# Kernel tuning notes

Measured on AMD Instinct MI355X. Metric: run time of the kernel, lower is better.

The kernel has to match this reference:

```python
import jax, jax.numpy as jnp
import numpy as np

HW = 8   # window height
WW = 8   # window width
NH = 8   # num heads
N = HW * WW  # tokens per window
DIM = 128
KEXPAND = 2


def _rel_index():
    # Swin relative-position index, [N, N] ints in [0, (2*HW-1)*(2*WW-1))
    coords = np.stack(np.meshgrid(np.arange(HW), np.arange(WW), indexing='ij')).reshape(2, -1)
    rel = (coords[:, :, None] - coords[:, None, :]).transpose(1, 2, 0)  # [N,N,2]
    rel[..., 0] += HW - 1
    rel[..., 1] += WW - 1
    rel[..., 0] *= 2 * WW - 1
    return jnp.asarray(rel.sum(-1))


def setup_inputs() -> dict:
    key = jax.random.key(0)
    ks = jax.random.split(key, 13)
    b, h, w, c = 4, 256, 256, DIM
    inp = {
        'qq': jax.random.normal(ks[0], (b, h * w, c), jnp.float32),
        'kk': jax.random.normal(ks[1], (b, h * w, KEXPAND * c), jnp.float32),
        'vv': jax.random.normal(ks[2], (b, h * w, c), jnp.float32),
        'w_q': jax.random.normal(ks[3], (c, c), jnp.float32) * 0.02,
        'b_q': jnp.zeros((c,), jnp.float32),
        'w_k': jax.random.normal(ks[4], (KEXPAND * c, c), jnp.float32) * 0.02,
        'b_k': jnp.zeros((c,), jnp.float32),
        'w_v': jax.random.normal(ks[5], (c, c), jnp.float32) * 0.02,
        'b_v': jnp.zeros((c,), jnp.float32),
        'w_o': jax.random.normal(ks[6], (c, c), jnp.float32) * 0.02,
        'b_o': jnp.zeros((c,), jnp.float32),
        'bias_table': jax.random.normal(ks[7], ((2 * HW - 1) * (2 * WW - 1), NH), jnp.float32) * 0.02,
        'h': h,
        'w': w,
    }
    return inp


def reference(qq, kk, vv, w_q, b_q, w_k, b_k, w_v, b_v, w_o, b_o, bias_table, h, w):
    b, n, c = qq.shape
    hd = c // NH
    pad_b = (-h) % HW
    pad_r = (-w) % WW
    Hp, Wp = h + pad_b, w + pad_r

    def pad_img(x):
        ck = x.shape[-1]
        x = x.reshape(b, h, w, ck)
        return jnp.pad(x, ((0, 0), (0, pad_b), (0, pad_r), (0, 0)))

    # QKV projections (zero-padded regions become just the bias, same as torch)
    qp = pad_img(qq) @ w_q + b_q  # [b, Hp, Wp, c]
    kp = pad_img(kk) @ w_k + b_k
    vp = pad_img(vv) @ w_v + b_v

    def windows(x):
        x = x.reshape(b, Hp // HW, HW, Wp // WW, WW, c)
        x = x.transpose(0, 1, 3, 2, 4, 5).reshape(-1, N, NH, hd)
        return x.transpose(0, 2, 1, 3)  # [nw, NH, N, hd]

    q, k, v = windows(qp), windows(kp), windows(vp)

    scores = jnp.einsum('wnqd,wnkd->wnqk', q, k) / jnp.sqrt(jnp.asarray(hd, q.dtype))
    bias = bias_table[_rel_index().reshape(-1)].reshape(N, N, NH).transpose(2, 0, 1)  # [NH,N,N]
    attn = jax.nn.softmax(scores + bias[None], axis=-1)
    y = jnp.einsum('wnqk,wnkd->wnqd', attn, v)  # [nw, NH, N, hd]

    # merge heads and un-window
    y = y.transpose(0, 2, 1, 3).reshape(b, Hp // HW, Wp // WW, HW, WW, c)
    y = y.transpose(0, 1, 3, 2, 4, 5).reshape(b, Hp, Wp, c)
    out = y @ w_o + b_o
    out = out[:, :h, :w, :]
    return out.reshape(b, -1, c)
```

## Files before the change

### kernel.cpp

```cpp
#include <hip/hip_runtime.h>
#include <cstdint>

typedef float f32x4  __attribute__((ext_vector_type(4)));
typedef float f32x16 __attribute__((ext_vector_type(16)));
typedef short bf16x8 __attribute__((ext_vector_type(8)));
typedef unsigned int u32;

#define QP_BASE 0
#define KP_BASE 16384
#define VT_BASE 32768

__device__ __forceinline__ unsigned short f2bf(float f){
  union { float f; uint32_t u; } v; v.f = f;
  uint32_t u = v.u;
  return (unsigned short)((u + 0x7FFFu + ((u >> 16) & 1u)) >> 16);
}
__device__ __forceinline__ float bf2f(unsigned short h){
  union { uint32_t u; float f; } v; v.u = ((uint32_t)h) << 16;
  return v.f;
}
__device__ __forceinline__ u32 pack2bf(float a, float b){
  return (u32)f2bf(a) | ((u32)f2bf(b) << 16);
}
__device__ __forceinline__ f32x4 mfma16(bf16x8 a, bf16x8 b, f32x4 c){
  return __builtin_amdgcn_mfma_f32_16x16x32_bf16(a, b, c, 0, 0, 0);
}
__device__ __forceinline__ f32x16 mfma32(bf16x8 a, bf16x8 b, f32x16 c){
  return __builtin_amdgcn_mfma_f32_32x32x16_bf16(a, b, c, 0, 0, 0);
}
__device__ __forceinline__ void gload_lds16(const void* gsrc, void* ldst){
  __builtin_amdgcn_global_load_lds(
    (const __attribute__((address_space(1))) unsigned int*)gsrc,
    (__attribute__((address_space(3))) unsigned int*)ldst, 16, 0, 0);
}

__global__ void prep_kernel(const float* __restrict__ wq, const float* __restrict__ wk,
                            const float* __restrict__ wv, const float* __restrict__ wo,
                            const float* __restrict__ btab, unsigned short* __restrict__ wsu)
{
  const int idx = blockIdx.x * 256 + threadIdx.x;
  if (idx < 16384){
    const int n = idx >> 7, k = idx & 127;
    wsu[n*128 + (k ^ ((n & 7) << 3))] = f2bf(wq[k*128 + n]);
  } else if (idx < 32768){
    const int i = idx - 16384, n = i >> 7, k = i & 127;
    wsu[16384 + n*128 + (k ^ ((n & 7) << 3))] = f2bf(wv[k*128 + n]);
  } else if (idx < 65536){
    const int i = idx - 32768, n = i >> 8, k = i & 255;
    wsu[32768 + n*256 + (k ^ ((n & 7) << 3))] = f2bf(wk[k*128 + n]);
  } else if (idx < 81920){
    const int i = idx - 65536, n = i >> 7, k = i & 127;
    const float f = wo[k*128 + n];
    const unsigned short hv = f2bf(f);
    wsu[65536 + n*128 + k] = hv;
    wsu[81920 + n*128 + k] = f2bf(f - bf2f(hv));
  } else if (idx < 98304){
    const int i = idx - 81920;
    const int q  = i & 31;
    const int ib = (i >> 5) & 7;
    const int h5 = (i >> 8) & 1;
    const int t  = (i >> 9) & 1;
    const int qh = (i >> 10) & 1;
    const int h  = (i >> 11);
    const int qg = qh*32 + q;
    const int qi = qg >> 3, qj = qg & 7;
    u32 wv2 = 0;
#pragma unroll
    for (int e = 0; e < 2; ++e){
      const int r = 2*ib + e;
      const int key = t*32 + 4*h5 + (r & 3) + 8*(r >> 2);
      const int ki = key >> 3, kj = key & 7;
      const int rel = (qi - ki + 7) * 15 + (qj - kj + 7);
      wv2 |= ((u32)f2bf(btab[rel*8 + h])) << (16*e);
    }
    reinterpret_cast<u32*>(wsu + 98304)[i] = wv2;
  }
}

template<int KC, bool VT>
__device__ __forceinline__ void proj_one(const float* __restrict__ X, const float* __restrict__ bias,
    const char* wlds, char* outstage, long winbase, int wave, int lane, int g, int c16)
{
  constexpr int NKS = KC / 32;
  constexpr int SH  = (KC == 128) ? 8 : 9;
  const int rA = 16*wave + c16;
  const float* xrow = X + (winbase + (long)(rA >> 3) * 256 + (rA & 7)) * KC;
  bf16x8 a[NKS];
#pragma unroll
  for (int ks = 0; ks < NKS; ++ks){
    const float4* p = reinterpret_cast<const float4*>(xrow + 32*ks + 8*g);
    const float4 x0 = p[0], x1 = p[1];
    bf16x8 t;
    t[0]=(short)f2bf(x0.x); t[1]=(short)f2bf(x0.y); t[2]=(short)f2bf(x0.z); t[3]=(short)f2bf(x0.w);
    t[4]=(short)f2bf(x1.x); t[5]=(short)f2bf(x1.y); t[6]=(short)f2bf(x1.z); t[7]=(short)f2bf(x1.w);
    a[ks] = t;
  }
  f32x4 acc[8];
#pragma unroll
  for (int ct = 0; ct < 8; ++ct) acc[ct] = f32x4{0.f,0.f,0.f,0.f};
#pragma unroll
  for (int ct = 0; ct < 8; ++ct){
    const int n = ct*16 + c16;
#pragma unroll
    for (int ks = 0; ks < NKS; ++ks){
      const bf16x8 b = *reinterpret_cast<const bf16x8*>(
          wlds + ((n << SH) + (((32*ks + 8*g) << 1) ^ ((n & 7) << 4))));
      acc[ct] = mfma16(a[ks], b, acc[ct]);
    }
  }
#pragma unroll
  for (int ct = 0; ct < 8; ++ct){
    const float bsv = bias[ct*16 + c16];
#pragma unroll
    for (int r = 0; r < 4; ++r){
      const float v = acc[ct][r] + bsv;
      const unsigned short hv = f2bf(v);
      const int row = 16*wave + 4*g + r;
      int off;
      if (VT) off = (ct << 11) + (c16 << 7) + ((row << 1) ^ ((c16 & 7) << 4));
      else    off = (row << 8) + (((ct*16 + c16) << 1) ^ ((row & 15) << 4));
      *reinterpret_cast<unsigned short*>(outstage + off) = hv;
    }
  }
}

__global__ __launch_bounds__(256, 2) void proj_kernel(
    const float* __restrict__ qq, const float* __restrict__ kkin, const float* __restrict__ vvin,
    const float* __restrict__ b_q, const float* __restrict__ b_k, const float* __restrict__ b_v,
    const unsigned short* __restrict__ wsu,
    unsigned short* __restrict__ qs, unsigned short* __restrict__ ksg, unsigned short* __restrict__ vsg)
{
  __shared__ char smem[81920];
  const int tid = threadIdx.x;
  const int wave = tid >> 6, lane = tid & 63;
  const int g = lane >> 4, c16 = lane & 15;
  const bool isK = blockIdx.x >= 256;
  char* outstage = smem + 65536;

  const char* wsrc = reinterpret_cast<const char*>(wsu) + (isK ? 65536 : 0);
#pragma unroll
  for (int i = 0; i < 16; ++i){
    const int off = (wave*16 + i) * 1024;
    gload_lds16(wsrc + off + lane*16, smem + off);
  }
  __syncthreads();

  const int w0 = (isK ? (blockIdx.x - 256) : blockIdx.x) * 16;
  for (int wl = 0; wl < 16; ++wl){
    const int win = w0 + wl;
    const int bb = win >> 10, wy = (win >> 5) & 31, wx = win & 31;
    const long winbase = (long)bb * 65536 + (long)wy * 2048 + wx * 8;

    if (!isK){
      proj_one<128,false>(qq, b_q, smem, outstage, winbase, wave, lane, g, c16);
      asm volatile("s_waitcnt lgkmcnt(0)" ::: "memory");
      {
        char* dst = reinterpret_cast<char*>(qs) + (size_t)win * 16384 + wave*4096;
        const char* srcs = outstage + wave*4096;
#pragma unroll
        for (int i = 0; i < 4; ++i){
          const uint4 d = *reinterpret_cast<const uint4*>(srcs + i*1024 + lane*16);
          *reinterpret_cast<uint4*>(dst + i*1024 + lane*16) = d;
        }
      }
      __syncthreads();
      proj_one<128,true>(vvin, b_v, smem + 32768, outstage, winbase, wave, lane, g, c16);
      __syncthreads();
      {
        char* dst = reinterpret_cast<char*>(vsg) + (size_t)win * 16384;
#pragma unroll
        for (int i = 0; i < 4; ++i){
          const uint4 d = *reinterpret_cast<const uint4*>(outstage + tid*16 + i*4096);
          *reinterpret_cast<uint4*>(dst + tid*16 + i*4096) = d;
        }
      }
      __syncthreads();
    } else {
      proj_one<256,false>(kkin, b_k, smem, outstage, winbase, wave, lane, g, c16);
      asm volatile("s_waitcnt lgkmcnt(0)" ::: "memory");
      {
        char* dst = reinterpret_cast<char*>(ksg) + (size_t)win * 16384 + wave*4096;
        const char* srcs = outstage + wave*4096;
#pragma unroll
        for (int i = 0; i < 4; ++i){
          const uint4 d = *reinterpret_cast<const uint4*>(srcs + i*1024 + lane*16);
          *reinterpret_cast<uint4*>(dst + i*1024 + lane*16) = d;
        }
      }
      __syncthreads();
    }
  }
}

__global__ __launch_bounds__(512, 4) void attn_kernel(
    const unsigned short* __restrict__ qs, const unsigned short* __restrict__ ksg,
    const unsigned short* __restrict__ vsg, const unsigned short* __restrict__ wsu,
    const float* __restrict__ b_o, float* __restrict__ out)
{
  __shared__ char smem[49152];
  const int tid = threadIdx.x;
  const int wave = tid >> 6, lane = tid & 63;
  const int l31 = lane & 31, h5 = lane >> 5;
  const int qh = wave & 1, hp = wave >> 1;

  const int win = blockIdx.x;
  const int bb = win >> 10, wy = (win >> 5) & 31, wx = win & 31;
  const long winbase = (long)bb * 65536 + (long)wy * 2048 + wx * 8;

  const u32* bias_u = reinterpret_cast<const u32*>(wsu + 98304);

  {
    const char* srcs[3] = {
      reinterpret_cast<const char*>(qs)  + (size_t)win * 16384,
      reinterpret_cast<const char*>(ksg) + (size_t)win * 16384,
      reinterpret_cast<const char*>(vsg) + (size_t)win * 16384 };
#pragma unroll
    for (int rg = 0; rg < 3; ++rg)
#pragma unroll
      for (int j = 0; j < 2; ++j){
        const int off = j*8192 + tid*16;
        gload_lds16(srcs[rg] + off, smem + rg*16384 + off);
      }
  }
  __syncthreads();

  f32x16 y[2];
#pragma unroll
  for (int hh = 0; hh < 2; ++hh){
    const int h = 2*hp + hh;
    const int chb = (h*16 + 8*h5) * 2;
    bf16x8 kf0, kf1, qf;
    { const int row = l31;
      kf0 = *reinterpret_cast<const bf16x8*>(smem + KP_BASE + (row<<8) + (chb ^ ((row&15)<<4))); }
    { const int row = 32 + l31;
      kf1 = *reinterpret_cast<const bf16x8*>(smem + KP_BASE + (row<<8) + (chb ^ ((row&15)<<4))); }
    { const int row = qh*32 + l31;
      qf  = *reinterpret_cast<const bf16x8*>(smem + QP_BASE + (row<<8) + (chb ^ ((row&15)<<4))); }
    f32x16 z = {};
    f32x16 s0 = mfma32(kf0, qf, z);
    f32x16 s1 = mfma32(kf1, qf, z);

    const u32* bb2 = bias_u + ((((h*2 + qh)*2 + 0)*2 + h5)*8)*32 + l31;
    float t[32];
#pragma unroll
    for (int i = 0; i < 8; ++i){
      const u32 w0 = bb2[i*32];
      const u32 w1 = bb2[512 + i*32];
      t[2*i]     = fmaf(s0[2*i],   0.25f, bf2f((unsigned short)(w0 & 0xffff)));
      t[2*i+1]   = fmaf(s0[2*i+1], 0.25f, bf2f((unsigned short)(w0 >> 16)));
      t[16+2*i]  = fmaf(s1[2*i],   0.25f, bf2f((unsigned short)(w1 & 0xffff)));
      t[17+2*i]  = fmaf(s1[2*i+1], 0.25f, bf2f((unsigned short)(w1 >> 16)));
    }
    float m = t[0];
#pragma unroll
    for (int r = 1; r < 32; ++r) m = fmaxf(m, t[r]);
    m = fmaxf(m, __shfl_xor(m, 32));
    float sum = 0.f;
#pragma unroll
    for (int r = 0; r < 32; ++r){ t[r] = __expf(t[r] - m); sum += t[r]; }
    sum += __shfl_xor(sum, 32);
    const float rs = 1.0f / sum;
    u32 pk0[8], pk1[8];
#pragma unroll
    for (int i = 0; i < 8; ++i){
      pk0[i] = pack2bf(t[2*i]*rs,    t[2*i+1]*rs);
      pk1[i] = pack2bf(t[16+2*i]*rs, t[17+2*i]*rs);
    }

    f32x16 yy = {};
    const int chr = l31 & 15;
#pragma unroll
    for (int m4 = 0; m4 < 4; ++m4){
      const int jb = 4*(m4 & 1);
      const u32 a0 = (m4 < 2) ? pk0[jb]   : pk1[jb];
      const u32 a1 = (m4 < 2) ? pk0[jb+1] : pk1[jb+1];
      const u32 a2 = (m4 < 2) ? pk0[jb+2] : pk1[jb+2];
      const u32 a3 = (m4 < 2) ? pk0[jb+3] : pk1[jb+3];
      const u32 s0w = (u32)__shfl_xor((int)a0, 32);
      const u32 s1w = (u32)__shfl_xor((int)a1, 32);
      const u32 s2w = (u32)__shfl_xor((int)a2, 32);
      const u32 s3w = (u32)__shfl_xor((int)a3, 32);
      union { u32 w[4]; bf16x8 v; } afu;
      afu.w[0] = h5 ? s2w : a0;
      afu.w[1] = h5 ? s3w : a1;
      afu.w[2] = h5 ? a2  : s0w;
      afu.w[3] = h5 ? a3  : s1w;
      const int kb = 32*m4 + 16*h5;
      const bf16x8 bv = *reinterpret_cast<const bf16x8*>(
          smem + VT_BASE + (h<<11) + (chr<<7) + (kb ^ ((chr & 7) << 4)));
      yy = mfma32(afu.v, bv, yy);
    }
    y[hh] = yy;
  }
  __syncthreads();

  if (l31 < 16){
#pragma unroll
    for (int hh = 0; hh < 2; ++hh){
      const int ch = (2*hp + hh)*16 + l31;
#pragma unroll
      for (int r = 0; r < 16; ++r){
        const int row = qh*32 + (r & 3) + 8*(r >> 2) + 4*h5;
        const float v = y[hh][r];
        const unsigned short hv = f2bf(v);
        const unsigned short lv = f2bf(v - bf2f(hv));
        const int byte = (row << 8) + ((ch << 1) ^ ((row & 15) << 4));
        *reinterpret_cast<unsigned short*>(smem + byte)         = hv;
        *reinterpret_cast<unsigned short*>(smem + 16384 + byte) = lv;
      }
    }
  }
  __syncthreads();

  {
    const int g = lane >> 4, c16 = lane & 15;
    const int ct = wave;
    const unsigned short* WT_oh = wsu + 65536;
    const unsigned short* WT_ol = wsu + 81920;
    bf16x8 bh[4], bl[4];
#pragma unroll
    for (int ks = 0; ks < 4; ++ks){
      bh[ks] = *reinterpret_cast<const bf16x8*>(WT_oh + (ct*16+c16)*128 + 32*ks + 8*g);
      bl[ks] = *reinterpret_cast<const bf16x8*>(WT_ol + (ct*16+c16)*128 + 32*ks + 8*g);
    }
    const float bov = b_o[ct*16 + c16];
#pragma unroll
    for (int rt = 0; rt < 4; ++rt){
      const int row2 = rt*16 + c16;
      bf16x8 ah[4], al[4];
#pragma unroll
      for (int ks = 0; ks < 4; ++ks){
        const int byte = (row2 << 8) + ((64*ks + 16*g) ^ ((row2 & 15) << 4));
        ah[ks] = *reinterpret_cast<const bf16x8*>(smem + byte);
        al[ks] = *reinterpret_cast<const bf16x8*>(smem + 16384 + byte);
      }
      f32x4 acc = {};
#pragma unroll
      for (int ks = 0; ks < 4; ++ks){
        acc = mfma16(ah[ks], bh[ks], acc);
        acc = mfma16(al[ks], bh[ks], acc);
        acc = mfma16(ah[ks], bl[ks], acc);
      }
#pragma unroll
      for (int r = 0; r < 4; ++r){
        const int R = rt*16 + 4*g + r;
        const long tok = winbase + (long)(R >> 3)*256 + (R & 7);
        out[tok*128 + ct*16 + c16] = acc[r] + bov;
      }
    }
  }
}

extern "C" void kernel_launch(void* const* d_in, const int* in_sizes, int n_in,
                              void* d_out, int out_size, void* d_ws, size_t ws_size,
                              hipStream_t stream)
{
  (void)in_sizes; (void)n_in; (void)out_size; (void)ws_size;
  const float* qq   = (const float*)d_in[0];
  const float* kk   = (const float*)d_in[1];
  const float* vv   = (const float*)d_in[2];
  const float* w_q  = (const float*)d_in[3];
  const float* b_q  = (const float*)d_in[4];
  const float* w_k  = (const float*)d_in[5];
  const float* b_k  = (const float*)d_in[6];
  const float* w_v  = (const float*)d_in[7];
  const float* b_v  = (const float*)d_in[8];
  const float* w_o  = (const float*)d_in[9];
  const float* b_o  = (const float*)d_in[10];
  const float* btab = (const float*)d_in[11];
  unsigned short* wsu = (unsigned short*)d_ws;
  float* out = (float*)d_out;

  unsigned short* qsp = wsu + 131072;
  unsigned short* ksp = qsp + 33554432;
  unsigned short* vsp = ksp + 33554432;

  prep_kernel<<<384, 256, 0, stream>>>(w_q, w_k, w_v, w_o, btab, wsu);
  proj_kernel<<<512, 256, 0, stream>>>(qq, kk, vv, b_q, b_k, b_v, wsu, qsp, ksp, vsp);
  attn_kernel<<<4096, 512, 0, stream>>>(qsp, ksp, vsp, wsu, b_o, out);
}
```

Measured before the change: 266.9 us.

## Split projection into per-tensor kernels with register prefetch of next window

The single projection kernel is split into three kernels (Q, V, K), each loading only its own weight into LDS. This cuts LDS footprint and allows more blocks per CU, with more blocks each handling fewer windows. Each block prefetches the next window's fp32 inputs into registers while the current window's MFMAs run. The V transposed output is now built with lane shuffles and written straight to global, skipping the LDS staging pass and its barriers. In exchange there are extra kernel launches, each block reloads weights for fewer windows, and register pressure rises.

Measured after the change: 310.7 us. +16.4%, slower.

```diff
diff --git a/kernel.cpp b/kernel.cpp
--- a/kernel.cpp
+++ b/kernel.cpp
@@ -77,119 +77,147 @@
   }
 }
 
-template<int KC, bool VT>
-__device__ __forceinline__ void proj_one(const float* __restrict__ X, const float* __restrict__ bias,
-    const char* wlds, char* outstage, long winbase, int wave, int lane, int g, int c16)
+template<int KC, int MODE>
+__device__ __forceinline__ void proj_body(const float* __restrict__ X,
+    const float* __restrict__ bias, const unsigned short* __restrict__ wbase_g,
+    unsigned short* __restrict__ outg, char* smem, int w0, int nwin)
 {
   constexpr int NKS = KC / 32;
   constexpr int SH  = (KC == 128) ? 8 : 9;
-  const int rA = 16*wave + c16;
-  const float* xrow = X + (winbase + (long)(rA >> 3) * 256 + (rA & 7)) * KC;
-  bf16x8 a[NKS];
-#pragma unroll
-  for (int ks = 0; ks < NKS; ++ks){
-    const float4* p = reinterpret_cast<const float4*>(xrow + 32*ks + 8*g);
-    const float4 x0 = p[0], x1 = p[1];
-    bf16x8 t;
-    t[0]=(short)f2bf(x0.x); t[1]=(short)f2bf(x0.y); t[2]=(short)f2bf(x0.z); t[3]=(short)f2bf(x0.w);
-    t[4]=(short)f2bf(x1.x); t[5]=(short)f2bf(x1.y); t[6]=(short)f2bf(x1.z); t[7]=(short)f2bf(x1.w);
-    a[ks] = t;
-  }
-  f32x4 acc[8];
-#pragma unroll
-  for (int ct = 0; ct < 8; ++ct) acc[ct] = f32x4{0.f,0.f,0.f,0.f};
-#pragma unroll
-  for (int ct = 0; ct < 8; ++ct){
-    const int n = ct*16 + c16;
-#pragma unroll
-    for (int ks = 0; ks < NKS; ++ks){
-      const bf16x8 b = *reinterpret_cast<const bf16x8*>(
-          wlds + ((n << SH) + (((32*ks + 8*g) << 1) ^ ((n & 7) << 4))));
-      acc[ct] = mfma16(a[ks], b, acc[ct]);
-    }
-  }
-#pragma unroll
-  for (int ct = 0; ct < 8; ++ct){
-    const float bsv = bias[ct*16 + c16];
-#pragma unroll
-    for (int r = 0; r < 4; ++r){
-      const float v = acc[ct][r] + bsv;
-      const unsigned short hv = f2bf(v);
-      const int row = 16*wave + 4*g + r;
-      int off;
-      if (VT) off = (ct << 11) + (c16 << 7) + ((row << 1) ^ ((c16 & 7) << 4));
-      else    off = (row << 8) + (((ct*16 + c16) << 1) ^ ((row & 15) << 4));
-      *reinterpret_cast<unsigned short*>(outstage + off) = hv;
-    }
-  }
-}
-
-__global__ __launch_bounds__(256, 2) void proj_kernel(
-    const float* __restrict__ qq, const float* __restrict__ kkin, const float* __restrict__ vvin,
-    const float* __restrict__ b_q, const float* __restrict__ b_k, const float* __restrict__ b_v,
-    const unsigned short* __restrict__ wsu,
-    unsigned short* __restrict__ qs, unsigned short* __restrict__ ksg, unsigned short* __restrict__ vsg)
-{
-  __shared__ char smem[81920];
+  constexpr int WBYTES = KC * 128 * 2;
   const int tid = threadIdx.x;
   const int wave = tid >> 6, lane = tid & 63;
   const int g = lane >> 4, c16 = lane & 15;
-  const bool isK = blockIdx.x >= 256;
-  char* outstage = smem + 65536;
-
-  const char* wsrc = reinterpret_cast<const char*>(wsu) + (isK ? 65536 : 0);
-#pragma unroll
-  for (int i = 0; i < 16; ++i){
-    const int off = (wave*16 + i) * 1024;
-    gload_lds16(wsrc + off + lane*16, smem + off);
-  }
+
+#pragma unroll
+  for (int i = 0; i < WBYTES/4096; ++i)
+    gload_lds16(reinterpret_cast<const char*>(wbase_g) + i*4096 + tid*16, smem + i*4096 + tid*16);
   __syncthreads();
-
-  const int w0 = (isK ? (blockIdx.x - 256) : blockIdx.x) * 16;
-  for (int wl = 0; wl < 16; ++wl){
+  char* outstage = smem + WBYTES;
+
+  float bias_r[8];
+#pragma unroll
+  for (int ct = 0; ct < 8; ++ct) bias_r[ct] = bias[ct*16 + c16];
+
+  const int rA = 16*wave + c16;
+  const int rowoff = ((rA >> 3) << 8) + (rA & 7);
+
+  float4 raw[2*NKS];
+  {
+    const int win = w0;
+    const long winbase = (long)(win >> 10)*65536 + (long)((win >> 5) & 31)*2048 + (win & 31)*8;
+    const float* xrow = X + (winbase + rowoff) * KC;
+#pragma unroll
+    for (int ks = 0; ks < NKS; ++ks){
+      const float4* p = reinterpret_cast<const float4*>(xrow + 32*ks + 8*g);
+      raw[2*ks] = p[0]; raw[2*ks+1] = p[1];
+    }
+  }
+
+  for (int wl = 0; wl < nwin; ++wl){
     const int win = w0 + wl;
-    const int bb = win >> 10, wy = (win >> 5) & 31, wx = win & 31;
-    const long winbase = (long)bb * 65536 + (long)wy * 2048 + wx * 8;
-
-    if (!isK){
-      proj_one<128,false>(qq, b_q, smem, outstage, winbase, wave, lane, g, c16);
+    bf16x8 a[NKS];
+#pragma unroll
+    for (int ks = 0; ks < NKS; ++ks){
+      const float4 x0 = raw[2*ks], x1 = raw[2*ks+1];
+      bf16x8 t;
+      t[0]=(short)f2bf(x0.x); t[1]=(short)f2bf(x0.y); t[2]=(short)f2bf(x0.z); t[3]=(short)f2bf(x0.w);
+      t[4]=(short)f2bf(x1.x); t[5]=(short)f2bf(x1.y); t[6]=(short)f2bf(x1.z); t[7]=(short)f2bf(x1.w);
+      a[ks] = t;
+    }
+    if (wl + 1 < nwin){
+      const int win2 = win + 1;
+      const long wb2 = (long)(win2 >> 10)*65536 + (long)((win2 >> 5) & 31)*2048 + (win2 & 31)*8;
+      const float* xrow2 = X + (wb2 + rowoff) * KC;
+#pragma unroll
+      for (int ks = 0; ks < NKS; ++ks){
+        const float4* p = reinterpret_cast<const float4*>(xrow2 + 32*ks + 8*g);
+        raw[2*ks] = p[0]; raw[2*ks+1] = p[1];
+      }
+    }
+    f32x4 acc[8];
+#pragma unroll
+    for (int ct = 0; ct < 8; ++ct) acc[ct] = f32x4{0.f,0.f,0.f,0.f};
+#pragma unroll
+    for (int ct = 0; ct < 8; ++ct){
+      const int n = ct*16 + c16;
+#pragma unroll
+      for (int ks = 0; ks < NKS; ++ks){
+        const bf16x8 b = *reinterpret_cast<const bf16x8*>(
+            smem + ((n << SH) + (((32*ks + 8*g) << 1) ^ ((n & 7) << 4))));
+        acc[ct] = mfma16(a[ks], b, acc[ct]);
+      }
+    }
+
+    if (MODE == 0){
+#pragma unroll
+      for (int ct = 0; ct < 8; ++ct){
+#pragma unroll
+        for (int r = 0; r < 4; ++r){
+          const int row = 16*wave + 4*g + r;
+          const int off = (row << 8) + (((ct*16 + c16) << 1) ^ ((row & 15) << 4));
+          *reinterpret_cast<unsigned short*>(outstage + off) = f2bf(acc[ct][r] + bias_r[ct]);
+        }
+      }
       asm volatile("s_waitcnt lgkmcnt(0)" ::: "memory");
-      {
-        char* dst = reinterpret_cast<char*>(qs) + (size_t)win * 16384 + wave*4096;
-        const char* srcs = outstage + wave*4096;
-#pragma unroll
-        for (int i = 0; i < 4; ++i){
-          const uint4 d = *reinterpret_cast<const uint4*>(srcs + i*1024 + lane*16);
-          *reinterpret_cast<uint4*>(dst + i*1024 + lane*16) = d;
-        }
-      }
-      __syncthreads();
-      proj_one<128,true>(vvin, b_v, smem + 32768, outstage, winbase, wave, lane, g, c16);
-      __syncthreads();
-      {
-        char* dst = reinterpret_cast<char*>(vsg) + (size_t)win * 16384;
-#pragma unroll
-        for (int i = 0; i < 4; ++i){
-          const uint4 d = *reinterpret_cast<const uint4*>(outstage + tid*16 + i*4096);
-          *reinterpret_cast<uint4*>(dst + tid*16 + i*4096) = d;
-        }
-      }
-      __syncthreads();
+      char* dst = reinterpret_cast<char*>(outg) + (size_t)win * 16384 + wave*4096;
+      const char* srcs = outstage + wave*4096;
+#pragma unroll
+      for (int i = 0; i < 4; ++i){
+        const uint4 d = *reinterpret_cast<const uint4*>(srcs + i*1024 + lane*16);
+        *reinterpret_cast<uint4*>(dst + i*1024 + lane*16) = d;
+      }
     } else {
-      proj_one<256,false>(kkin, b_k, smem, outstage, winbase, wave, lane, g, c16);
-      asm volatile("s_waitcnt lgkmcnt(0)" ::: "memory");
-      {
-        char* dst = reinterpret_cast<char*>(ksg) + (size_t)win * 16384 + wave*4096;
-        const char* srcs = outstage + wave*4096;
-#pragma unroll
-        for (int i = 0; i < 4; ++i){
-          const uint4 d = *reinterpret_cast<const uint4*>(srcs + i*1024 + lane*16);
-          *reinterpret_cast<uint4*>(dst + i*1024 + lane*16) = d;
-        }
-      }
-      __syncthreads();
-    }
-  }
+      u32 pa[8], pb[8];
+#pragma unroll
+      for (int ct = 0; ct < 8; ++ct){
+        const float v0 = acc[ct][0] + bias_r[ct], v1 = acc[ct][1] + bias_r[ct];
+        const float v2 = acc[ct][2] + bias_r[ct], v3 = acc[ct][3] + bias_r[ct];
+        pa[ct] = pack2bf(v0, v1); pb[ct] = pack2bf(v2, v3);
+      }
+      const int p  = g & 1;
+      const int kk = g >> 1;
+      const int t  = 2*wave + kk;
+      u32 sa[4], sb[4];
+#pragma unroll
+      for (int i = 0; i < 4; ++i){
+        const int cs = p ? i : 4 + i;
+        sa[i] = (u32)__shfl_xor((int)pa[cs], 16);
+        sb[i] = (u32)__shfl_xor((int)pb[cs], 16);
+      }
+      char* wout = reinterpret_cast<char*>(outg) + (size_t)win * 16384;
+#pragma unroll
+      for (int i = 0; i < 4; ++i){
+        const int ct2 = 4*p + i;
+        uint4 chunk;
+        if (p == 0){ chunk.x = pa[ct2]; chunk.y = pb[ct2]; chunk.z = sa[i]; chunk.w = sb[i]; }
+        else       { chunk.x = sa[i];   chunk.y = sb[i];   chunk.z = pa[ct2]; chunk.w = pb[ct2]; }
+        *reinterpret_cast<uint4*>(wout + ct2*2048 + c16*128 + 16*(t ^ (c16 & 7))) = chunk;
+      }
+    }
+  }
+}
+
+__global__ __launch_bounds__(256, 3) void proj_q(const float* __restrict__ qq,
+    const float* __restrict__ b_q, const unsigned short* __restrict__ wsu,
+    unsigned short* __restrict__ qs)
+{
+  __shared__ char smem[49152];
+  proj_body<128,0>(qq, b_q, wsu, qs, smem, blockIdx.x*4, 4);
+}
+__global__ __launch_bounds__(256, 3) void proj_v(const float* __restrict__ vv,
+    const float* __restrict__ b_v, const unsigned short* __restrict__ wsu,
+    unsigned short* __restrict__ vsg)
+{
+  __shared__ char smem[32768];
+  proj_body<128,1>(vv, b_v, wsu + 16384, vsg, smem, blockIdx.x*4, 4);
+}
+__global__ __launch_bounds__(256, 2) void proj_k(const float* __restrict__ kkin,
+    const float* __restrict__ b_k, const unsigned short* __restrict__ wsu,
+    unsigned short* __restrict__ ksg)
+{
+  __shared__ char smem[81920];
+  proj_body<256,0>(kkin, b_k, wsu + 32768, ksg, smem, blockIdx.x*8, 8);
 }
 
 __global__ __launch_bounds__(512, 4) void attn_kernel(
@@ -376,6 +404,8 @@
   unsigned short* vsp = ksp + 33554432;
 
   prep_kernel<<<384, 256, 0, stream>>>(w_q, w_k, w_v, w_o, btab, wsu);
-  proj_kernel<<<512, 256, 0, stream>>>(qq, kk, vv, b_q, b_k, b_v, wsu, qsp, ksp, vsp);
+  proj_q<<<1024, 256, 0, stream>>>(qq, b_q, wsu, qsp);
+  proj_v<<<1024, 256, 0, stream>>>(vv, b_v, wsu, vsp);
+  proj_k<<<512,  256, 0, stream>>>(kk, b_k, wsu, ksp);
   attn_kernel<<<4096, 512, 0, stream>>>(qsp, ksp, vsp, wsu, b_o, out);
 }
```
